# Performance work log

Measured on AMD Instinct MI355X. Metric: run time of the kernel, lower is better.

Reference implementation:

```python
import jax, jax.numpy as jnp
import numpy as np

P = 8      # patch_size
DIM = 16   # per-head channel dim
HEADS = 4
LN_EPS = 1e-6


def _conv_patch(x, W, b):
    # stride=kernel=P patch conv; SAME degenerates to VALID when H%P==0
    y = jax.lax.conv_general_dilated(
        x, W, window_strides=(P, P), padding='VALID',
        dimension_numbers=('NHWC', 'HWIO', 'NHWC'))
    return y + b


def _proj_heads(x, W, b):
    # b h w (c p0 p1 head) -> b head (h p0) (w p1) c
    y = _conv_patch(x, W, b)
    B, hh, ww, _ = y.shape
    y = y.reshape(B, hh, ww, DIM, P, P, HEADS)
    y = y.transpose(0, 6, 1, 4, 2, 5, 3)            # b head hh p0 ww p1 c
    return y.reshape(B, HEADS, hh * P, ww * P, DIM)


def _to_patch(t):
    # n head (h p1) (w p2) c -> n head c h w p1 p2
    B, hd, H, W, c = t.shape
    t = t.reshape(B, hd, H // P, P, W // P, P, c)
    return t.transpose(0, 1, 6, 2, 4, 3, 5)


def _from_patch(t):
    # n head c h w p1 p2 -> n head (h p1) (w p2) c
    B, hd, c, hh, ww, _, _ = t.shape
    t = t.transpose(0, 1, 3, 5, 4, 6, 2)
    return t.reshape(B, hd, hh * P, ww * P, c)


def setup_inputs() -> dict:
    key = jax.random.key(0)
    ks = jax.random.split(key, 6)
    B, H, W, Cin = 4, 256, 256, 16
    feat = DIM * HEADS * P * P  # 4096
    s_qkv = 0.02
    inp = {
        'x': jax.random.normal(ks[0], (B, H, W, Cin), jnp.float32),
        'Wq': jax.random.normal(ks[1], (P, P, Cin, feat), jnp.float32) * s_qkv,
        'bq': jnp.zeros((feat,), jnp.float32),
        'Wk': jax.random.normal(ks[2], (P, P, Cin, feat), jnp.float32) * s_qkv,
        'bk': jnp.zeros((feat,), jnp.float32),
        'Wv': jax.random.normal(ks[3], (P, P, Cin, feat), jnp.float32) * s_qkv,
        'bv': jnp.zeros((feat,), jnp.float32),
        'ln_scale': jnp.ones((DIM,), jnp.float32),
        'ln_bias': jnp.zeros((DIM,), jnp.float32),
        'Wout': jax.random.normal(ks[4], (P, P, HEADS * DIM, DIM * P * P), jnp.float32) * 0.02,
        'bout': jnp.zeros((DIM * P * P,), jnp.float32),
    }
    return inp


def reference(x, Wq, bq, Wk, bk, Wv, bv, ln_scale, ln_bias, Wout, bout):
    q = _proj_heads(x, Wq, bq)  # [B, heads, H, W, dim]
    k = _proj_heads(x, Wk, bk)
    v = _proj_heads(x, Wv, bv)

    # frequency-domain 'attention': per-8x8-patch rfft2 multiply irfft2
    qf = jnp.fft.rfft2(_to_patch(q))
    kf = jnp.fft.rfft2(_to_patch(k))
    out = jnp.fft.irfft2(qf * kf, s=(P, P))
    out = _from_patch(out)                          # [B, heads, H, W, dim]

    # LayerNorm over channel dim (flax default eps=1e-6, scale+bias)
    mu = out.mean(-1, keepdims=True)
    var = ((out - mu) ** 2).mean(-1, keepdims=True)
    out = (out - mu) * jax.lax.rsqrt(var + LN_EPS) * ln_scale + ln_bias

    out = v * out
    # b head h w c -> b h w (head c)
    B, hd, H, W, c = out.shape
    out = out.transpose(0, 2, 3, 1, 4).reshape(B, H, W, hd * c)

    # output projection (no heads): conv then b h w (c p0 p1) -> b (h p0) (w p1) c
    y = _conv_patch(out, Wout, bout)
    Bo, hh, ww, _ = y.shape
    y = y.reshape(Bo, hh, ww, DIM, P, P).transpose(0, 1, 4, 2, 5, 3)
    return y.reshape(Bo, hh * P, ww * P, DIM)
```

## Files before the change

kernel.cpp:

```cpp
#include <hip/hip_runtime.h>
#include <hip/hip_bf16.h>
#include <cstdint>
#include <cstddef>

typedef float  f32x4  __attribute__((ext_vector_type(4)));
typedef __bf16 bf16x8 __attribute__((ext_vector_type(8)));
typedef __bf16 bf16x4 __attribute__((ext_vector_type(4)));


#define GLOAD_LDS16(gp, lp)                                                     \
    __builtin_amdgcn_global_load_lds(                                           \
        (const __attribute__((address_space(1))) void*)(gp),                    \
        (__attribute__((address_space(3))) void*)(lp), 16, 0, 0)

#define MFMA16(d, a, b) d = __builtin_amdgcn_mfma_f32_16x16x32_bf16(a, b, d, 0, 0, 0)

__global__ __launch_bounds__(256) void k_im2col(const float* __restrict__ x,
                                                __bf16* __restrict__ Xb)
{
    const int p = blockIdx.x;
    const int t = threadIdx.x;
    const int b = p >> 10, hh = (p >> 5) & 31, ww = p & 31;
    const int e = t * 4;
    const int c = e & 15, ij = e >> 4;
    const int i = ij >> 3, j = ij & 7;
    const size_t src = ((((size_t)(b * 256 + hh * 8 + i)) * 256) + (ww * 8 + j)) * 16 + c;
    f32x4 v = *(const f32x4*)(x + src);
    bf16x4 o;
    o[0] = (__bf16)v[0]; o[1] = (__bf16)v[1]; o[2] = (__bf16)v[2]; o[3] = (__bf16)v[3];
    *(bf16x4*)(Xb + (size_t)p * 1024 + e) = o;
}

__global__ __launch_bounds__(256) void k_wqkvT(const float* __restrict__ Wq,
                                               const float* __restrict__ Wk,
                                               const float* __restrict__ Wv,
                                               __bf16* __restrict__ WT)
{
    __shared__ float tile[64][261];
    int q = blockIdx.x;
    const int t = threadIdx.x;
    const int kb = q & 15;   q >>= 4;
    const int ch = q & 15;   q >>= 4;
    const int s  = q;
    const int k0 = kb * 64;
    const float* __restrict__ W = (s == 0) ? Wq : (s == 1) ? Wk : Wv;

#pragma unroll
    for (int rep = 0; rep < 16; rep++) {
        const int idx = rep * 256 + t;
        const int kl = idx >> 6, col4 = (idx & 63) * 4;
        const f32x4 v = *(const f32x4*)(W + (size_t)(k0 + kl) * 4096 + ch * 256 + col4);
        tile[kl][col4 + 0] = v[0];
        tile[kl][col4 + 1] = v[1];
        tile[kl][col4 + 2] = v[2];
        tile[kl][col4 + 3] = v[3];
    }
    __syncthreads();
    const size_t nbase = (size_t)s * 4096 + ch * 64;
#pragma unroll
    for (int rep = 0; rep < 64; rep++) {
        const int idx = rep * 256 + t;
        const int kl = idx & 63;
        const int rest = idx >> 6;
        const int p = rest & 63, h = rest >> 6;
        WT[(nbase + h * 1024 + p) * 1024 + k0 + kl] = (__bf16)tile[kl][p * 4 + h];
    }
}

__global__ __launch_bounds__(256) void k_biasperm(const float* __restrict__ bq,
                                                  const float* __restrict__ bk,
                                                  const float* __restrict__ bv,
                                                  float* __restrict__ bp)
{
    const int n = blockIdx.x * 256 + threadIdx.x;
    const int s = n >> 12;
    const int r = n & 4095;
    const int head = r >> 10, c = (r >> 6) & 15, pp = r & 63;
    const float* __restrict__ b = (s == 0) ? bq : (s == 1) ? bk : bv;
    bp[n] = b[c * 256 + pp * 4 + head];
}

__global__ __launch_bounds__(256) void k_woutT(const float* __restrict__ Wo,
                                               __bf16* __restrict__ WT)
{
    __shared__ float tile[64][129];
    const int q = blockIdx.x;
    const int t = threadIdx.x;
    const int n0 = (q & 15) * 64;
    const int k0 = (q >> 4) * 128;
    const int ch = n0 >> 6;
#pragma unroll
    for (int rep = 0; rep < 32; rep++) {
        const int idx = rep * 256 + t;
        const int kl = idx >> 6, nn = idx & 63;
        tile[nn][kl] = Wo[(size_t)(k0 + kl) * 1024 + n0 + nn];
    }
    __syncthreads();
#pragma unroll
    for (int rep = 0; rep < 32; rep++) {
        const int idx = rep * 256 + t;
        const int nn = idx >> 7, kl = idx & 127;
        const int no = ((nn >> 3) & 7) * 128 + (nn & 7) * 16 + ch;
        WT[(size_t)no * 4096 + k0 + kl] = (__bf16)tile[nn][kl];
    }
}

__device__ __forceinline__ void stage_half(const __bf16* __restrict__ mat,
                                           const int gRow0, const int K,
                                           const int k0, __bf16* lds, const int t)
{
    const int w6 = (t >> 6) << 6;
#pragma unroll
    for (int r = 0; r < 2; r++) {
        const int idx = r * 512 + t;
        const int row = idx >> 3;
        const int colb = ((t & 7) << 4) ^ ((row & 7) << 4);
        const char* gp = (const char*)(mat + (size_t)(gRow0 + row) * K + k0) + colb;
        GLOAD_LDS16(gp, (char*)lds + (size_t)(r * 512 + w6) * 16);
    }
}

__global__ __launch_bounds__(512, 1) void gemm256(const __bf16* __restrict__ A,
                                                  const __bf16* __restrict__ Bt,
                                                  __bf16* __restrict__ C,
                                                  const float* __restrict__ bias,
                                                  const int M, const int N,
                                                  const int K, const int nby)
{
    __shared__ __bf16 As[2][256 * 64];
    __shared__ __bf16 Bs[2][256 * 64];

    const int t = threadIdx.x;
    const int l = t & 63, w = t >> 6;
    const int wr = w >> 2, wc = w & 3;

    const int nwg = (int)gridDim.x, cpx = nwg >> 3;
    const int bid = (int)blockIdx.x;
    const int sbid = (bid & 7) * cpx + (bid >> 3);
    const int bm = sbid % nby, bn = sbid / nby;
    const int row0 = bm * 256, col0 = bn * 256;

    const int lrow = l & 15;
    const int lkb  = (l >> 4) << 4;
    const int lswz = (l & 7) << 4;
    const int ce0 = ((0  + lkb) ^ lswz) >> 1;
    const int ce1 = ((64 + lkb) ^ lswz) >> 1;

    const int arow = wr * 128 + lrow;
    const int brow = wc * 64 + lrow;

    const int NT = K >> 6;
    f32x4 acc[8][4] = {};

    stage_half(A,  row0,       K, 0,  As[0],        t);
    stage_half(A,  row0 + 128, K, 0,  As[0] + 8192, t);
    stage_half(Bt, col0,       K, 0,  Bs[0],        t);
    stage_half(Bt, col0 + 128, K, 0,  Bs[0] + 8192, t);
    stage_half(A,  row0,       K, 64, As[1],        t);
    stage_half(A,  row0 + 128, K, 64, As[1] + 8192, t);
    asm volatile("s_waitcnt vmcnt(4)" ::: "memory");
    __builtin_amdgcn_s_barrier();

    int cur = 0;
    for (int it = 0; it < NT; ++it) {
        const __bf16* AsC = As[cur];
        const __bf16* BsC = Bs[cur];
        const bool doB = (it + 1 < NT);
        const bool doA = (it + 2 < NT);
        const int kB = (it + 1) << 6;
        const int kA = (it + 2) << 6;

        bf16x8 af[4][2], bfr[2][2];

#pragma unroll
        for (int mi = 0; mi < 4; ++mi) {
            const int rr = (arow + mi * 16) * 64;
            af[mi][0] = *(const bf16x8*)&AsC[rr + ce0];
            af[mi][1] = *(const bf16x8*)&AsC[rr + ce1];
        }
#pragma unroll
        for (int ni = 0; ni < 2; ++ni) {
            const int rr = (brow + ni * 16) * 64;
            bfr[ni][0] = *(const bf16x8*)&BsC[rr + ce0];
            bfr[ni][1] = *(const bf16x8*)&BsC[rr + ce1];
        }
        if (doB) stage_half(Bt, col0, K, kB, Bs[cur ^ 1], t);
        __builtin_amdgcn_s_barrier();
        __builtin_amdgcn_s_setprio(1);
#pragma unroll
        for (int mi = 0; mi < 4; ++mi)
#pragma unroll
            for (int ni = 0; ni < 2; ++ni) {
                MFMA16(acc[mi][ni], af[mi][0], bfr[ni][0]);
                MFMA16(acc[mi][ni], af[mi][1], bfr[ni][1]);
            }
        __builtin_amdgcn_s_setprio(0);
        __builtin_amdgcn_s_barrier();

#pragma unroll
        for (int ni = 0; ni < 2; ++ni) {
            const int rr = (brow + 32 + ni * 16) * 64;
            bfr[ni][0] = *(const bf16x8*)&BsC[rr + ce0];
            bfr[ni][1] = *(const bf16x8*)&BsC[rr + ce1];
        }
        if (doB) stage_half(Bt, col0 + 128, K, kB, Bs[cur ^ 1] + 8192, t);
        __builtin_amdgcn_s_barrier();
        __builtin_amdgcn_s_setprio(1);
#pragma unroll
        for (int mi = 0; mi < 4; ++mi)
#pragma unroll
            for (int ni = 0; ni < 2; ++ni) {
                MFMA16(acc[mi][2 + ni], af[mi][0], bfr[ni][0]);
                MFMA16(acc[mi][2 + ni], af[mi][1], bfr[ni][1]);
            }
        __builtin_amdgcn_s_setprio(0);
        __builtin_amdgcn_s_barrier();

#pragma unroll
        for (int mi = 0; mi < 4; ++mi) {
            const int rr = (arow + 64 + mi * 16) * 64;
            af[mi][0] = *(const bf16x8*)&AsC[rr + ce0];
            af[mi][1] = *(const bf16x8*)&AsC[rr + ce1];
        }
#pragma unroll
        for (int ni = 0; ni < 2; ++ni) {
            const int rr = (brow + ni * 16) * 64;
            bfr[ni][0] = *(const bf16x8*)&BsC[rr + ce0];
            bfr[ni][1] = *(const bf16x8*)&BsC[rr + ce1];
        }
        __builtin_amdgcn_s_barrier();
        __builtin_amdgcn_s_setprio(1);
#pragma unroll
        for (int mi = 0; mi < 4; ++mi)
#pragma unroll
            for (int ni = 0; ni < 2; ++ni) {
                MFMA16(acc[4 + mi][ni], af[mi][0], bfr[ni][0]);
                MFMA16(acc[4 + mi][ni], af[mi][1], bfr[ni][1]);
            }
        __builtin_amdgcn_s_setprio(0);
        __builtin_amdgcn_s_barrier();

        if (doA) {
            stage_half(A, row0,       K, kA, As[cur],        t);
            stage_half(A, row0 + 128, K, kA, As[cur] + 8192, t);
        }
#pragma unroll
        for (int ni = 0; ni < 2; ++ni) {
            const int rr = (brow + 32 + ni * 16) * 64;
            bfr[ni][0] = *(const bf16x8*)&BsC[rr + ce0];
            bfr[ni][1] = *(const bf16x8*)&BsC[rr + ce1];
        }
        __builtin_amdgcn_s_barrier();
        __builtin_amdgcn_s_setprio(1);
#pragma unroll
        for (int mi = 0; mi < 4; ++mi)
#pragma unroll
            for (int ni = 0; ni < 2; ++ni) {
                MFMA16(acc[4 + mi][2 + ni], af[mi][0], bfr[ni][0]);
                MFMA16(acc[4 + mi][2 + ni], af[mi][1], bfr[ni][1]);
            }
        __builtin_amdgcn_s_setprio(0);
        if (it + 1 < NT) {
            if (doA) asm volatile("s_waitcnt vmcnt(4)" ::: "memory");
            else     asm volatile("s_waitcnt vmcnt(0)" ::: "memory");
            __builtin_amdgcn_s_barrier();
        }
        cur ^= 1;
    }

    const int rbase = row0 + wr * 128;
    const int cbase = col0 + wc * 64;
    const int jr = (l >> 4) * 4;
#pragma unroll
    for (int m = 0; m < 8; ++m)
#pragma unroll
        for (int n = 0; n < 4; ++n) {
            const int cw = cbase + n * 16 + lrow;
            const float bsv = bias[cw];
#pragma unroll
            for (int j = 0; j < 4; ++j) {
                const int rw = rbase + m * 16 + jr + j;
                C[(size_t)rw * N + cw] = (__bf16)(acc[m][n][j] + bsv);
            }
        }
}

template <int BN, int EPI>
__global__ __launch_bounds__(256, 3) void gemm_glds(const __bf16* __restrict__ A,
                                                    const __bf16* __restrict__ Bt,
                                                    void* __restrict__ Cout,
                                                    const float* __restrict__ bias,
                                                    const int M, const int N,
                                                    const int K, const int nbx)
{
    constexpr int BM  = 128, BK = 64;
    constexpr int NF  = BN / 32;
    constexpr int APW = (BM * BK / 512) / 4;
    constexpr int BPW = (BN * BK / 512) / 4;
    __shared__ __bf16 As[BM * BK];
    __shared__ __bf16 Bs[BN * BK];

    const int t = threadIdx.x;
    const int l = t & 63, w = t >> 6;

    const int nwg  = (int)gridDim.x;
    const int cpx  = nwg >> 3;
    const int bid  = (int)blockIdx.x;
    const int sbid = (bid & 7) * cpx + (bid >> 3);
    const int bm = sbid / nbx, bn = sbid - bm * nbx;
    const int row0 = bm * BM, col0 = bn * BN;

    const int wr = w >> 1, wc = w & 1;
    const int lr = l & 15;
    const int lk = (l >> 4) * 8;
    const int srow = l >> 3;
    const int scol = (l & 7) * 8;

    f32x4 acc[4][NF] = {};

    for (int k0 = 0; k0 < K; k0 += BK) {
        __syncthreads();
#pragma unroll
        for (int p = 0; p < APW; p++) {
            const int chunk = w * APW + p;
            const __bf16* gp = A + (size_t)(row0 + chunk * 8 + srow) * K + k0 + scol;
            GLOAD_LDS16(gp, &As[chunk * 512]);
        }
#pragma unroll
        for (int p = 0; p < BPW; p++) {
            const int chunk = w * BPW + p;
            const __bf16* gp = Bt + (size_t)(col0 + chunk * 8 + srow) * K + k0 + scol;
            GLOAD_LDS16(gp, &Bs[chunk * 512]);
        }
        __syncthreads();
#pragma unroll
        for (int kk = 0; kk < 2; kk++) {
            bf16x8 af[4], bfr[NF];
#pragma unroll
            for (int m = 0; m < 4; m++)
                af[m] = *(const bf16x8*)&As[(wr * 64 + m * 16 + lr) * BK + kk * 32 + lk];
#pragma unroll
            for (int n = 0; n < NF; n++)
                bfr[n] = *(const bf16x8*)&Bs[(wc * (BN / 2) + n * 16 + lr) * BK + kk * 32 + lk];
#pragma unroll
            for (int m = 0; m < 4; m++)
#pragma unroll
                for (int n = 0; n < NF; n++)
                    acc[m][n] = __builtin_amdgcn_mfma_f32_16x16x32_bf16(
                        af[m], bfr[n], acc[m][n], 0, 0, 0);
        }
    }

    const int rbase = row0 + wr * 64;
    const int cbase = col0 + wc * (BN / 2);
    if (EPI == 0) {
        __bf16* __restrict__ C = (__bf16*)Cout;
#pragma unroll
        for (int m = 0; m < 4; m++)
#pragma unroll
            for (int n = 0; n < NF; n++) {
                const int cw = cbase + n * 16 + lr;
                const float bsv = bias[cw];
#pragma unroll
                for (int j = 0; j < 4; j++) {
                    const int rw = rbase + m * 16 + (l >> 4) * 4 + j;
                    C[(size_t)rw * N + cw] = (__bf16)(acc[m][n][j] + bsv);
                }
            }
    } else {
        float* __restrict__ Y = (float*)Cout;
#pragma unroll
        for (int m = 0; m < 4; m++)
#pragma unroll
            for (int n = 0; n < NF; n++) {
                const int cw = cbase + n * 16 + lr;
                const float bsv = bias[((cw & 15) << 6) + ((cw >> 7) << 3) + ((cw >> 4) & 7)];
                const int p0 = cw >> 7, low = cw & 127;
#pragma unroll
                for (int j = 0; j < 4; j++) {
                    const int rw = rbase + m * 16 + (l >> 4) * 4 + j;
                    const int b = rw >> 10, hh = (rw >> 5) & 31, wwp = rw & 31;
                    const size_t addr =
                        (size_t)(b * 256 + hh * 8 + p0) * 4096 + wwp * 128 + low;
                    Y[addr] = acc[m][n][j] + bsv;
                }
            }
    }
}

__global__ __launch_bounds__(128) void k_freqconv(const __bf16* __restrict__ C1,
                                                  const float* __restrict__ lns,
                                                  const float* __restrict__ lnb,
                                                  __bf16* __restrict__ Z)
{
    const int blk = blockIdx.x;
    const int p = blk >> 2, head = blk & 3;
    const int t = threadIdx.x;

    __shared__ float qs[16 * 68];
    __shared__ float ks[16 * 68];
    __shared__ float vs[16 * 68];
    __shared__ float os[16 * 68];

    const __bf16* __restrict__ base = C1 + (size_t)p * 12288 + head * 1024;
    {
        const int cl = t >> 3, off = (t & 7) * 8;
        const bf16x8 vq = *(const bf16x8*)(base + cl * 64 + off);
        const bf16x8 vk = *(const bf16x8*)(base + 4096 + cl * 64 + off);
        const bf16x8 vv = *(const bf16x8*)(base + 8192 + cl * 64 + off);
#pragma unroll
        for (int e = 0; e < 8; e++) {
            qs[cl * 68 + off + e] = (float)vq[e];
            ks[cl * 68 + off + e] = (float)vk[e];
            vs[cl * 68 + off + e] = (float)vv[e];
        }
    }
    __syncthreads();

    const int cc = t >> 3, p0 = t & 7;
    float outr[8] = {0.f, 0.f, 0.f, 0.f, 0.f, 0.f, 0.f, 0.f};
#pragma unroll
    for (int i0 = 0; i0 < 8; i0++) {
        const int kr = (p0 - i0) & 7;
        const f32x4 qa = *(const f32x4*)&qs[cc * 68 + i0 * 8];
        const f32x4 qb = *(const f32x4*)&qs[cc * 68 + i0 * 8 + 4];
        const f32x4 ka = *(const f32x4*)&ks[cc * 68 + kr * 8];
        const f32x4 kb = *(const f32x4*)&ks[cc * 68 + kr * 8 + 4];
        const float qrow[8] = {qa[0], qa[1], qa[2], qa[3], qb[0], qb[1], qb[2], qb[3]};
        const float krow[8] = {ka[0], ka[1], ka[2], ka[3], kb[0], kb[1], kb[2], kb[3]};
#pragma unroll
        for (int j = 0; j < 8; j++) {
            const float qv = qrow[j];
#pragma unroll
            for (int p1 = 0; p1 < 8; p1++)
                outr[p1] = fmaf(qv, krow[(p1 - j) & 7], outr[p1]);
        }
    }
#pragma unroll
    for (int e = 0; e < 8; e++)
        os[cc * 68 + p0 * 8 + e] = outr[e];
    __syncthreads();

    if (t < 64) {
        const int pp = t;
        float o[16];
        float mu = 0.f;
#pragma unroll
        for (int c2 = 0; c2 < 16; c2++) { o[c2] = os[c2 * 68 + pp]; mu += o[c2]; }
        mu *= 0.0625f;
        float var = 0.f;
#pragma unroll
        for (int c2 = 0; c2 < 16; c2++) { const float d = o[c2] - mu; var = fmaf(d, d, var); }
        var *= 0.0625f;
        const float rs = rsqrtf(var + 1e-6f);
        bf16x8 z0, z1;
#pragma unroll
        for (int c2 = 0; c2 < 16; c2++) {
            float zv = (o[c2] - mu) * rs * lns[c2] + lnb[c2];
            zv *= vs[c2 * 68 + pp];
            if (c2 < 8) z0[c2] = (__bf16)zv; else z1[c2 - 8] = (__bf16)zv;
        }
        bf16x8* zp = (bf16x8*)(Z + (size_t)p * 4096 + pp * 64 + head * 16);
        zp[0] = z0;
        zp[1] = z1;
    }
}

extern "C" void kernel_launch(void* const* d_in, const int* in_sizes, int n_in,
                              void* d_out, int out_size, void* d_ws, size_t ws_size,
                              hipStream_t stream)
{
    const float* x   = (const float*)d_in[0];
    const float* Wq  = (const float*)d_in[1];
    const float* bq  = (const float*)d_in[2];
    const float* Wk  = (const float*)d_in[3];
    const float* bk  = (const float*)d_in[4];
    const float* Wv  = (const float*)d_in[5];
    const float* bv  = (const float*)d_in[6];
    const float* lns = (const float*)d_in[7];
    const float* lnb = (const float*)d_in[8];
    const float* Wo  = (const float*)d_in[9];
    const float* bo  = (const float*)d_in[10];
    float* out = (float*)d_out;

    char* ws = (char*)d_ws;
    __bf16* Xb    = (__bf16*)(ws);
    __bf16* WqkvT = (__bf16*)(ws + 8388608);
    float*  bperm = (float*) (ws + 33554432);
    __bf16* WoutT = (__bf16*)(ws + 33603584);
    __bf16* C1    = (__bf16*)(ws + 41992192);
    __bf16* Z     = (__bf16*)(ws + 142655488);

    k_im2col  <<<dim3(4096), dim3(256), 0, stream>>>(x, Xb);
    k_wqkvT   <<<dim3(768),  dim3(256), 0, stream>>>(Wq, Wk, Wv, WqkvT);
    k_biasperm<<<dim3(48),   dim3(256), 0, stream>>>(bq, bk, bv, bperm);
    k_woutT   <<<dim3(512),  dim3(256), 0, stream>>>(Wo, WoutT);

    gemm256<<<dim3(768), dim3(512), 0, stream>>>(Xb, WqkvT, C1, bperm,
                                                 4096, 12288, 1024, 16);

    k_freqconv<<<dim3(16384), dim3(128), 0, stream>>>(C1, lns, lnb, Z);

    gemm_glds<128, 1><<<dim3(256), dim3(256), 0, stream>>>(Z, WoutT, (void*)out, bo,
                                                           4096, 1024, 4096, 8);
}
```

Baseline: 258.2 us.

## Restructure GEMM main loop with double-buffered register fragments and cross-iteration A prefetch

The main GEMM loop now keeps separate register sets for both A halves and both B halves. All B fragments and the second A half are loaded up front, and the first A half for the next iteration is prefetched from the other LDS buffer during the current iteration's MFMA phases. Barriers and vmcnt waits are rearranged so LDS reads overlap MFMA work with fewer stalls between phases. The cost is higher register pressure (more live bf16x8 fragments), and the tighter barrier and waitcnt placement carries a risk of subtle synchronization hazards.

```diff
diff --git a/kernel.cpp b/kernel.cpp
--- a/kernel.cpp
+++ b/kernel.cpp
@@ -14,6 +14,8 @@
         (__attribute__((address_space(3))) void*)(lp), 16, 0, 0)
 
 #define MFMA16(d, a, b) d = __builtin_amdgcn_mfma_f32_16x16x32_bf16(a, b, d, 0, 0, 0)
+
+#define BAR() asm volatile("s_barrier" ::: "memory")
 
 __global__ __launch_bounds__(256) void k_im2col(const float* __restrict__ x,
                                                 __bf16* __restrict__ Xb)
@@ -151,120 +153,115 @@
 
     const int NT = K >> 6;
     f32x4 acc[8][4] = {};
+    bf16x8 a0[4][2], a1[4][2], b0[2][2], b1[2][2];
 
     stage_half(A,  row0,       K, 0,  As[0],        t);
     stage_half(A,  row0 + 128, K, 0,  As[0] + 8192, t);
+    stage_half(A,  row0,       K, 64, As[1],        t);
+    stage_half(A,  row0 + 128, K, 64, As[1] + 8192, t);
     stage_half(Bt, col0,       K, 0,  Bs[0],        t);
     stage_half(Bt, col0 + 128, K, 0,  Bs[0] + 8192, t);
-    stage_half(A,  row0,       K, 64, As[1],        t);
-    stage_half(A,  row0 + 128, K, 64, As[1] + 8192, t);
-    asm volatile("s_waitcnt vmcnt(4)" ::: "memory");
-    __builtin_amdgcn_s_barrier();
+    asm volatile("s_waitcnt vmcnt(0)" ::: "memory");
+    BAR();
+#pragma unroll
+    for (int mi = 0; mi < 4; ++mi) {
+        const int rr = (arow + mi * 16) * 64;
+        a0[mi][0] = *(const bf16x8*)&As[0][rr + ce0];
+        a0[mi][1] = *(const bf16x8*)&As[0][rr + ce1];
+    }
 
     int cur = 0;
     for (int it = 0; it < NT; ++it) {
         const __bf16* AsC = As[cur];
+        const __bf16* AsN = As[cur ^ 1];
         const __bf16* BsC = Bs[cur];
-        const bool doB = (it + 1 < NT);
-        const bool doA = (it + 2 < NT);
+        __bf16* BsN = Bs[cur ^ 1];
+        const bool stB = (it + 1 < NT);
+        const bool stA = (it + 2 < NT);
+        const bool pfA = (it + 1 < NT);
         const int kB = (it + 1) << 6;
         const int kA = (it + 2) << 6;
 
-        bf16x8 af[4][2], bfr[2][2];
-
-#pragma unroll
-        for (int mi = 0; mi < 4; ++mi) {
-            const int rr = (arow + mi * 16) * 64;
-            af[mi][0] = *(const bf16x8*)&AsC[rr + ce0];
-            af[mi][1] = *(const bf16x8*)&AsC[rr + ce1];
-        }
+        BAR();
 #pragma unroll
         for (int ni = 0; ni < 2; ++ni) {
             const int rr = (brow + ni * 16) * 64;
-            bfr[ni][0] = *(const bf16x8*)&BsC[rr + ce0];
-            bfr[ni][1] = *(const bf16x8*)&BsC[rr + ce1];
-        }
-        if (doB) stage_half(Bt, col0, K, kB, Bs[cur ^ 1], t);
-        __builtin_amdgcn_s_barrier();
-        __builtin_amdgcn_s_setprio(1);
-#pragma unroll
-        for (int mi = 0; mi < 4; ++mi)
-#pragma unroll
-            for (int ni = 0; ni < 2; ++ni) {
-                MFMA16(acc[mi][ni], af[mi][0], bfr[ni][0]);
-                MFMA16(acc[mi][ni], af[mi][1], bfr[ni][1]);
-            }
-        __builtin_amdgcn_s_setprio(0);
-        __builtin_amdgcn_s_barrier();
-
+            b0[ni][0] = *(const bf16x8*)&BsC[rr + ce0];
+            b0[ni][1] = *(const bf16x8*)&BsC[rr + ce1];
+        }
 #pragma unroll
         for (int ni = 0; ni < 2; ++ni) {
             const int rr = (brow + 32 + ni * 16) * 64;
-            bfr[ni][0] = *(const bf16x8*)&BsC[rr + ce0];
-            bfr[ni][1] = *(const bf16x8*)&BsC[rr + ce1];
-        }
-        if (doB) stage_half(Bt, col0 + 128, K, kB, Bs[cur ^ 1] + 8192, t);
-        __builtin_amdgcn_s_barrier();
-        __builtin_amdgcn_s_setprio(1);
-#pragma unroll
-        for (int mi = 0; mi < 4; ++mi)
-#pragma unroll
-            for (int ni = 0; ni < 2; ++ni) {
-                MFMA16(acc[mi][2 + ni], af[mi][0], bfr[ni][0]);
-                MFMA16(acc[mi][2 + ni], af[mi][1], bfr[ni][1]);
-            }
-        __builtin_amdgcn_s_setprio(0);
-        __builtin_amdgcn_s_barrier();
-
+            b1[ni][0] = *(const bf16x8*)&BsC[rr + ce0];
+            b1[ni][1] = *(const bf16x8*)&BsC[rr + ce1];
+        }
 #pragma unroll
         for (int mi = 0; mi < 4; ++mi) {
             const int rr = (arow + 64 + mi * 16) * 64;
-            af[mi][0] = *(const bf16x8*)&AsC[rr + ce0];
-            af[mi][1] = *(const bf16x8*)&AsC[rr + ce1];
-        }
-#pragma unroll
-        for (int ni = 0; ni < 2; ++ni) {
-            const int rr = (brow + ni * 16) * 64;
-            bfr[ni][0] = *(const bf16x8*)&BsC[rr + ce0];
-            bfr[ni][1] = *(const bf16x8*)&BsC[rr + ce1];
-        }
-        __builtin_amdgcn_s_barrier();
+            a1[mi][0] = *(const bf16x8*)&AsC[rr + ce0];
+            a1[mi][1] = *(const bf16x8*)&AsC[rr + ce1];
+        }
+        if (stB) stage_half(Bt, col0, K, kB, BsN, t);
         __builtin_amdgcn_s_setprio(1);
 #pragma unroll
         for (int mi = 0; mi < 4; ++mi)
 #pragma unroll
             for (int ni = 0; ni < 2; ++ni) {
-                MFMA16(acc[4 + mi][ni], af[mi][0], bfr[ni][0]);
-                MFMA16(acc[4 + mi][ni], af[mi][1], bfr[ni][1]);
+                MFMA16(acc[mi][ni], a0[mi][0], b0[ni][0]);
+                MFMA16(acc[mi][ni], a0[mi][1], b0[ni][1]);
             }
         __builtin_amdgcn_s_setprio(0);
-        __builtin_amdgcn_s_barrier();
-
-        if (doA) {
+
+        BAR();
+        if (stB) stage_half(Bt, col0 + 128, K, kB, BsN + 8192, t);
+        __builtin_amdgcn_s_setprio(1);
+#pragma unroll
+        for (int mi = 0; mi < 4; ++mi)
+#pragma unroll
+            for (int ni = 0; ni < 2; ++ni) {
+                MFMA16(acc[mi][2 + ni], a0[mi][0], b1[ni][0]);
+                MFMA16(acc[mi][2 + ni], a0[mi][1], b1[ni][1]);
+            }
+        __builtin_amdgcn_s_setprio(0);
+        asm volatile("s_waitcnt vmcnt(4)" ::: "memory");
+
+        BAR();
+        if (pfA) {
+#pragma unroll
+            for (int mi = 0; mi < 4; ++mi) {
+                const int rr = (arow + mi * 16) * 64;
+                a0[mi][0] = *(const bf16x8*)&AsN[rr + ce0];
+                a0[mi][1] = *(const bf16x8*)&AsN[rr + ce1];
+            }
+        }
+        __builtin_amdgcn_s_setprio(1);
+#pragma unroll
+        for (int mi = 0; mi < 4; ++mi)
+#pragma unroll
+            for (int ni = 0; ni < 2; ++ni) {
+                MFMA16(acc[4 + mi][ni], a1[mi][0], b0[ni][0]);
+                MFMA16(acc[4 + mi][ni], a1[mi][1], b0[ni][1]);
+            }
+        __builtin_amdgcn_s_setprio(0);
+
+        BAR();
+        if (stA) {
             stage_half(A, row0,       K, kA, As[cur],        t);
             stage_half(A, row0 + 128, K, kA, As[cur] + 8192, t);
-        }
-#pragma unroll
-        for (int ni = 0; ni < 2; ++ni) {
-            const int rr = (brow + 32 + ni * 16) * 64;
-            bfr[ni][0] = *(const bf16x8*)&BsC[rr + ce0];
-            bfr[ni][1] = *(const bf16x8*)&BsC[rr + ce1];
-        }
-        __builtin_amdgcn_s_barrier();
+            asm volatile("s_waitcnt vmcnt(4)" ::: "memory");
+        } else {
+            asm volatile("s_waitcnt vmcnt(0)" ::: "memory");
+        }
         __builtin_amdgcn_s_setprio(1);
 #pragma unroll
         for (int mi = 0; mi < 4; ++mi)
 #pragma unroll
             for (int ni = 0; ni < 2; ++ni) {
-                MFMA16(acc[4 + mi][2 + ni], af[mi][0], bfr[ni][0]);
-                MFMA16(acc[4 + mi][2 + ni], af[mi][1], bfr[ni][1]);
+                MFMA16(acc[4 + mi][2 + ni], a1[mi][0], b1[ni][0]);
+                MFMA16(acc[4 + mi][2 + ni], a1[mi][1], b1[ni][1]);
             }
         __builtin_amdgcn_s_setprio(0);
-        if (it + 1 < NT) {
-            if (doA) asm volatile("s_waitcnt vmcnt(4)" ::: "memory");
-            else     asm volatile("s_waitcnt vmcnt(0)" ::: "memory");
-            __builtin_amdgcn_s_barrier();
-        }
+
         cur ^= 1;
     }
 
```

Result: faster. 251.5 us (-2.6%).
